# Optimization experiments

Measured on AMD Instinct MI355X. Metric: run time of the kernel, lower is better.

## Reference

```python
import jax, jax.numpy as jnp
import numpy as np

MODES = 32
WIDTH = 64


def crelu(z):
    # split-complex ReLU (torch.relu is undefined on complex; this is the standard fix)
    return jax.nn.relu(z.real) + 1j * jax.nn.relu(z.imag)


def _linear_params(key, fan_in, fan_out):
    k1, k2 = jax.random.split(key)
    s = 1.0 / np.sqrt(fan_in)
    W = jax.random.uniform(k1, (fan_out, fan_in), minval=-s, maxval=s, dtype=jnp.float32)
    b = jax.random.uniform(k2, (fan_out,), minval=-s, maxval=s, dtype=jnp.float32)
    return W, b


def setup_inputs() -> dict:
    key = jax.random.key(0)
    ks = jax.random.split(key, 8)
    B, G = 32768, 512
    H0, H1, H2 = 1024, 512, 64  # hidden_layers; H2 == WIDTH
    FD = 128                    # field_dim
    geometry_input = jax.random.normal(ks[0], (B, G), dtype=jnp.float32)
    W_in, b_in = _linear_params(ks[1], G, H0)
    W_h1, b_h1 = _linear_params(ks[2], H0, H1)
    W_h2, b_h2 = _linear_params(ks[3], H1, H2)
    w0 = jax.random.normal(ks[4], (MODES, WIDTH), dtype=jnp.float32)
    w1 = jax.random.normal(ks[5], (MODES, WIDTH), dtype=jnp.float32)
    lin1_W, lin1_b = _linear_params(ks[6], WIDTH, WIDTH)
    k7a, k7b = jax.random.split(ks[7])
    lin2_W, lin2_b = _linear_params(k7a, WIDTH, WIDTH)
    W_out, b_out = _linear_params(k7b, H2, FD)
    return dict(geometry_input=geometry_input, W_in=W_in, b_in=b_in,
                W_h1=W_h1, b_h1=b_h1, W_h2=W_h2, b_h2=b_h2,
                w0=w0, w1=w1, lin1_W=lin1_W, lin1_b=lin1_b,
                lin2_W=lin2_W, lin2_b=lin2_b, W_out=W_out, b_out=b_out)


def reference(geometry_input, W_in, b_in, W_h1, b_h1, W_h2, b_h2,
              w0, w1, lin1_W, lin1_b, lin2_W, lin2_b, W_out, b_out):
    # MLP encoder: [B, G] -> [B, 64]
    x = jax.nn.relu(geometry_input @ W_in.T + b_in)
    x = jax.nn.relu(x @ W_h1.T + b_h1)
    x = jax.nn.relu(x @ W_h2.T + b_h2)
    # FNO block
    xh = jnp.fft.fftn(x)  # fftn over ALL axes, as in torch code -> complex64 [B, 64]
    phase = jnp.exp(1j * 2.0 * jnp.pi * jnp.arange(MODES) / MODES).astype(jnp.complex64)
    y = xh[:, None, :] * w0  # per-mode lift: [B, MODES, WIDTH]
    y = crelu(y)
    y = y * phase[None, :, None]  # diagonal L mode-multiply
    y = jnp.einsum('bmw,mw->bw', y, w1.astype(y.dtype))  # collapse modes -> [B, WIDTH]
    y = crelu(y @ lin1_W.T + lin1_b)  # real weights on complex acts
    y = y @ lin2_W.T + lin2_b
    y = jnp.fft.ifftn(y)  # [B, 64] complex
    out = y @ W_out.T + b_out  # [B, field_dim] complex
    return out
```

## Files before the change

### kernel.cpp

```cpp
#include <hip/hip_runtime.h>
#include <hip/hip_bf16.h>


#define PI2F 6.28318530717958647692f

typedef __attribute__((ext_vector_type(8))) short short8;
typedef __attribute__((ext_vector_type(4))) float f32x4;

__device__ __forceinline__ unsigned short f2bf(float f) {
  unsigned int u = __float_as_uint(f);
  u += 0x7fff + ((u >> 16) & 1);
  return (unsigned short)(u >> 16);
}
__device__ __forceinline__ unsigned int pack_bf16x2(float a, float b) {
  return (unsigned int)f2bf(a) | ((unsigned int)f2bf(b) << 16);
}

__device__ __forceinline__ void gl2lds16(const void* gptr, const void* lptr) {
  __builtin_amdgcn_global_load_lds(
      (const __attribute__((address_space(1))) unsigned int*)(unsigned long long)gptr,
      (__attribute__((address_space(3))) unsigned int*)(unsigned int)(unsigned long long)lptr,
      16, 0, 0);
}

__global__ __launch_bounds__(256) void f32_to_bf16_k(
    const float* __restrict__ src, unsigned short* __restrict__ dst, int n4)
{
  int i = blockIdx.x * 256 + threadIdx.x;
  if (i < n4) {
    float4 v = ((const float4*)src)[i];
    uint2 p;
    p.x = pack_bf16x2(v.x, v.y);
    p.y = pack_bf16x2(v.z, v.w);
    ((uint2*)dst)[i] = p;
  }
}

template<int NBLOG, typename OUT>
__global__ __launch_bounds__(512, 1) void gemm_pipe(
    const unsigned short* __restrict__ A, const unsigned short* __restrict__ Bw,
    const float* __restrict__ bias, OUT* __restrict__ C, int N, int K)
{
  constexpr int BM = 128, BN = 256, BK = 64;
  constexpr int ASZ = BM * BK;
  constexpr int BSZ = BN * BK;
  constexpr int BUF = ASZ + BSZ;
  __shared__ __align__(16) unsigned short lds[3 * BUF];

  const int nwg = gridDim.x;
  const int cpx = nwg >> 3;
  const int orig = blockIdx.x;
  const int wg = (orig & 7) * cpx + (orig >> 3);
  const int mb = wg >> NBLOG;
  const int nb = wg & ((1 << NBLOG) - 1);
  const size_t m0 = (size_t)mb * BM;
  const size_t n0 = (size_t)nb * BN;

  const int tid = threadIdx.x;
  const int lane = tid & 63;
  const int wv = tid >> 6;
  const int q = lane >> 4, lr = lane & 15;
  const int x7 = lr & 7;
  const int wm = (wv >> 2) * 64;
  const int wn = (wv & 3) * 64;
  f32x4 acc[4][4] = {};

  auto STAGE_HALF = [&](int r, int kk, int s0) {
    unsigned short* dA = lds + r * BUF;
    #pragma unroll
    for (int u = 0; u < 3; ++u) {
      int e = wv * 6 + s0 + u;
      int isA = (e < 16) ? 1 : 0;
      int e2 = isA ? e : e - 16;
      int pc = e2 * 64 + lane;
      int row = pc >> 3, col = pc & 7;
      int lc = col ^ (row & 7);
      const unsigned short* src = isA ? A : Bw;
      size_t rb = isA ? m0 : n0;
      unsigned short* dst = dA + (isA ? 0 : ASZ) + e2 * 512;
      gl2lds16(src + (rb + row) * (size_t)K + kk + lc * 8, dst);
    }
  };

  const int nt = K / BK;
  STAGE_HALF(0, 0, 0); STAGE_HALF(0, 0, 3);
  STAGE_HALF(1, BK, 0); STAGE_HALF(1, BK, 3);
  asm volatile("s_waitcnt vmcnt(6)" ::: "memory");
  __builtin_amdgcn_s_barrier();

  int r0 = 0;
  for (int t = 0; t < nt; ++t) {
    const unsigned short* sA = lds + r0 * BUF;
    const unsigned short* sB = sA + ASZ;
    const bool st = (t + 2) < nt;
    const int r2 = (r0 >= 1) ? (r0 - 1) : 2;
    const int kk2 = (t + 2) * BK;

    short8 af[4][2], bf0[2][2];
    #pragma unroll
    for (int i = 0; i < 4; ++i)
      #pragma unroll
      for (int t2 = 0; t2 < 2; ++t2)
        af[i][t2] = *(const short8*)(sA + (wm + i * 16 + lr) * 64 + (((t2 << 2) | q) ^ x7) * 8);
    #pragma unroll
    for (int j = 0; j < 2; ++j)
      #pragma unroll
      for (int t2 = 0; t2 < 2; ++t2)
        bf0[j][t2] = *(const short8*)(sB + (wn + j * 16 + lr) * 64 + (((t2 << 2) | q) ^ x7) * 8);
    if (st) STAGE_HALF(r2, kk2, 0);
    __builtin_amdgcn_s_setprio(1);
    #pragma unroll
    for (int i = 0; i < 4; ++i)
      #pragma unroll
      for (int j = 0; j < 2; ++j)
        #pragma unroll
        for (int t2 = 0; t2 < 2; ++t2)
          acc[i][j] = __builtin_amdgcn_mfma_f32_16x16x32_bf16(af[i][t2], bf0[j][t2], acc[i][j], 0, 0, 0);
    __builtin_amdgcn_s_setprio(0);
    __builtin_amdgcn_s_barrier();

    short8 bf1[2][2];
    #pragma unroll
    for (int j = 0; j < 2; ++j)
      #pragma unroll
      for (int t2 = 0; t2 < 2; ++t2)
        bf1[j][t2] = *(const short8*)(sB + (wn + (j + 2) * 16 + lr) * 64 + (((t2 << 2) | q) ^ x7) * 8);
    if (st) STAGE_HALF(r2, kk2, 3);
    __builtin_amdgcn_s_setprio(1);
    #pragma unroll
    for (int i = 0; i < 4; ++i)
      #pragma unroll
      for (int j = 0; j < 2; ++j)
        #pragma unroll
        for (int t2 = 0; t2 < 2; ++t2)
          acc[i][j + 2] = __builtin_amdgcn_mfma_f32_16x16x32_bf16(af[i][t2], bf1[j][t2], acc[i][j + 2], 0, 0, 0);
    __builtin_amdgcn_s_setprio(0);

    asm volatile("s_waitcnt lgkmcnt(0)" ::: "memory");
    if (st) { asm volatile("s_waitcnt vmcnt(6)" ::: "memory"); }
    else    { asm volatile("s_waitcnt vmcnt(0)" ::: "memory"); }
    __builtin_amdgcn_s_barrier();
    r0 = (r0 + 1 >= 3) ? 0 : r0 + 1;
  }

  #pragma unroll
  for (int i = 0; i < 4; ++i)
    #pragma unroll
    for (int j = 0; j < 4; ++j) {
      size_t col = n0 + wn + j * 16 + lr;
      float bv = bias[col];
      #pragma unroll
      for (int r = 0; r < 4; ++r) {
        size_t row = m0 + wm + i * 16 + q * 4 + r;
        float v = acc[i][j][r] + bv;
        v = v > 0.f ? v : 0.f;
        if (sizeof(OUT) == 2) ((unsigned short*)C)[row * N + col] = f2bf(v);
        else                  ((float*)C)[row * N + col] = v;
      }
    }
}

template<int BM, int BN, int WM, int WN, typename OUT>
__global__ __launch_bounds__(256) void gemm_async(
    const unsigned short* __restrict__ A, const unsigned short* __restrict__ Bw,
    const float* __restrict__ bias, OUT* __restrict__ C,
    int M, int N, int K)
{
  constexpr int BK = 64;
  __shared__ __align__(16) unsigned short lA[BM * BK];
  __shared__ __align__(16) unsigned short lB[BN * BK];
  const int tid = threadIdx.x;
  const int lane = tid & 63;
  const int wv = tid >> 6;
  const int q = lane >> 4, lr = lane & 15;
  const int x7 = lr & 7;
  constexpr int WN_CNT = BN / WN;
  const int wm = (wv / WN_CNT) * WM;
  const int wn = (wv % WN_CNT) * WN;
  const size_t m0 = (size_t)blockIdx.x * BM;
  const size_t n0 = (size_t)blockIdx.y * BN;
  constexpr int MI = WM / 16, NI = WN / 16;
  f32x4 acc[MI][NI] = {};
  constexpr int A_INSTR = BM * BK / 512;
  constexpr int B_INSTR = BN * BK / 512;
  constexpr int A_PW = A_INSTR / 4, B_PW = B_INSTR / 4;
  (void)M;

  for (int k0 = 0; k0 < K; k0 += BK) {
    __syncthreads();
    #pragma unroll
    for (int s = 0; s < A_PW; ++s) {
      int instr = wv * A_PW + s;
      int pc = instr * 64 + lane;
      int row = pc >> 3, col = pc & 7;
      int lc = col ^ (row & 7);
      gl2lds16(A + (m0 + row) * K + k0 + lc * 8, lA + instr * 512);
    }
    #pragma unroll
    for (int s = 0; s < B_PW; ++s) {
      int instr = wv * B_PW + s;
      int pc = instr * 64 + lane;
      int row = pc >> 3, col = pc & 7;
      int lc = col ^ (row & 7);
      gl2lds16(Bw + (n0 + row) * K + k0 + lc * 8, lB + instr * 512);
    }
    __syncthreads();
    #pragma unroll
    for (int t = 0; t < 2; ++t) {
      short8 af[MI], bfr[NI];
      #pragma unroll
      for (int i = 0; i < MI; ++i) {
        int r = wm + i * 16 + lr;
        af[i] = *(const short8*)(lA + r * 64 + (((t << 2) | q) ^ x7) * 8);
      }
      #pragma unroll
      for (int j = 0; j < NI; ++j) {
        int r = wn + j * 16 + lr;
        bfr[j] = *(const short8*)(lB + r * 64 + (((t << 2) | q) ^ x7) * 8);
      }
      #pragma unroll
      for (int i = 0; i < MI; ++i)
        #pragma unroll
        for (int j = 0; j < NI; ++j)
          acc[i][j] = __builtin_amdgcn_mfma_f32_16x16x32_bf16(af[i], bfr[j], acc[i][j], 0, 0, 0);
    }
  }
  #pragma unroll
  for (int i = 0; i < MI; ++i)
    #pragma unroll
    for (int j = 0; j < NI; ++j) {
      size_t col = n0 + wn + j * 16 + lr;
      float bv = bias[col];
      #pragma unroll
      for (int r = 0; r < 4; ++r) {
        size_t row = m0 + wm + i * 16 + q * 4 + r;
        float v = acc[i][j][r] + bv;
        v = v > 0.f ? v : 0.f;
        if (sizeof(OUT) == 2) ((unsigned short*)C)[row * N + col] = f2bf(v);
        else                  ((float*)C)[row * N + col] = v;
      }
    }
}

__global__ __launch_bounds__(256) void precompute(
    const float* __restrict__ w0, const float* __restrict__ w1,
    const float* __restrict__ l2W, const float* __restrict__ l2b,
    float2* __restrict__ Ap, float2* __restrict__ Am,
    float2* __restrict__ Qt, float2* __restrict__ b2c)
{
  const int t = threadIdx.x;
  const int blk = blockIdx.x;
  if (blk == 0) {
    if (t < 64) {
      float apx = 0, apy = 0, amx = 0, amy = 0;
      for (int m = 0; m < 32; ++m) {
        float s0 = w0[m * 64 + t];
        float cf = w1[m * 64 + t] * s0;
        float sn, cs; sincosf(PI2F * (float)m / 32.f, &sn, &cs);
        if (s0 > 0.f)      { apx += cs * cf; apy += sn * cf; }
        else if (s0 < 0.f) { amx += cs * cf; amy += sn * cf; }
      }
      Ap[t] = make_float2(apx, apy);
      Am[t] = make_float2(amx, amy);
      float bx = 0, by = 0;
      for (int k = 0; k < 64; ++k) {
        float sn, cs; sincosf(PI2F * (float)((t * k) & 63) / 64.f, &sn, &cs);
        float lb = l2b[k] * (1.f / 64.f);
        bx += cs * lb; by += sn * lb;
      }
      b2c[t] = make_float2(bx, by);
    }
  } else {
    int e = (blk - 1) * 256 + t;
    int j = e >> 6, w = e & 63;
    float qx = 0, qy = 0;
    for (int k = 0; k < 64; ++k) {
      float sn, cs; sincosf(PI2F * (float)((j * k) & 63) / 64.f, &sn, &cs);
      float lw = l2W[k * 64 + w] * (1.f / 64.f);
      qx += cs * lw; qy += sn * lw;
    }
    Qt[w * 64 + j] = make_float2(qx, qy);
  }
}

__global__ __launch_bounds__(256) void dft64_rows(
    const float* __restrict__ x3, float2* __restrict__ xh1)
{
  __shared__ __align__(16) float xt[32][64];
  __shared__ float2 tw[64];
  const int t = threadIdx.x;
  const size_t b0 = (size_t)blockIdx.x * 32;
  for (int it = 0; it < 8; ++it) {
    int idx = it * 256 + t;
    int r = idx >> 6, w = idx & 63;
    xt[r][w] = x3[(b0 + r) * 64 + w];
  }
  if (t < 64) {
    float sn, cs; sincosf(-PI2F * (float)t / 64.f, &sn, &cs);
    tw[t] = make_float2(cs, sn);
  }
  __syncthreads();
  const int k = t & 63, rg = t >> 6;
  float2 acc[8] = {};
  #pragma unroll 1
  for (int w4 = 0; w4 < 16; ++w4) {
    int w = 4 * w4;
    int kw = k * w;
    float2 t0 = tw[kw & 63];
    float2 t1 = tw[(kw + k) & 63];
    float2 t2 = tw[(kw + 2 * k) & 63];
    float2 t3 = tw[(kw + 3 * k) & 63];
    #pragma unroll
    for (int r = 0; r < 8; ++r) {
      float4 xv = *(const float4*)(&xt[rg * 8 + r][w]);
      acc[r].x += xv.x * t0.x + xv.y * t1.x + xv.z * t2.x + xv.w * t3.x;
      acc[r].y += xv.x * t0.y + xv.y * t1.y + xv.z * t2.y + xv.w * t3.y;
    }
  }
  #pragma unroll
  for (int r = 0; r < 8; ++r)
    xh1[(b0 + rg * 8 + r) * 64 + k] = acc[r];
}

template<int SIGN>
__global__ __launch_bounds__(256) void fft_stage1(
    const float2* __restrict__ Xin, float2* __restrict__ T)
{
  __shared__ __align__(16) float2 tile[128 * 34];
  __shared__ float2 tw16s[16];
  const int blk = blockIdx.x;
  const int b2 = blk >> 1, wh = (blk & 1) * 32;
  const int t = threadIdx.x;
  #pragma unroll
  for (int it = 0; it < 8; ++it) {
    int idx = it * 256 + t;
    int b1 = idx >> 4, wi = (idx & 15) * 2;
    float4 v = *(const float4*)&Xin[((size_t)(b1 * 256 + b2)) * 64 + wh + wi];
    *(float4*)&tile[b1 * 34 + wi] = v;
  }
  if (t < 16) {
    float sn, cs; sincosf(SIGN * PI2F * (float)t / 16.f, &sn, &cs);
    tw16s[t] = make_float2(cs, sn);
  }
  __syncthreads();
  float2 twr[16];
  #pragma unroll
  for (int j = 0; j < 16; ++j) twr[j] = tw16s[j];

  {
    const int n2a = t >> 5, w = t & 31;
    float2 d[16];
    #pragma unroll
    for (int n1 = 0; n1 < 16; ++n1)
      d[n1] = tile[(8 * n1 + n2a) * 34 + w];
    float2 y[16];
    #pragma unroll
    for (int k = 0; k < 16; ++k) {
      float2 a = d[0];
      #pragma unroll
      for (int n1 = 1; n1 < 16; ++n1) {
        float2 tv = twr[(n1 * k) & 15];
        a.x += d[n1].x * tv.x - d[n1].y * tv.y;
        a.y += d[n1].x * tv.y + d[n1].y * tv.x;
      }
      y[k] = a;
    }
    float sstep, cstep;
    sincosf(SIGN * PI2F * (float)n2a / 128.f, &sstep, &cstep);
    float2 rot = make_float2(1.f, 0.f);
    #pragma unroll
    for (int k = 0; k < 16; ++k) {
      float2 a = y[k];
      y[k] = make_float2(a.x * rot.x - a.y * rot.y, a.x * rot.y + a.y * rot.x);
      float nrx = rot.x * cstep - rot.y * sstep;
      rot.y = rot.x * sstep + rot.y * cstep;
      rot.x = nrx;
    }
    __syncthreads();
    #pragma unroll
    for (int k = 0; k < 16; ++k)
      tile[(n2a * 16 + k) * 34 + w] = y[k];
  }
  __syncthreads();

  const int wB = t & 31, qB = t >> 5;
  float sstep, cstep;
  sincosf(SIGN * PI2F * (float)(16 * b2) / 32768.f, &sstep, &cstep);
  #pragma unroll
  for (int h = 0; h < 2; ++h) {
    const int k1p = qB + 8 * h;
    float2 d[8];
    #pragma unroll
    for (int n2 = 0; n2 < 8; ++n2)
      d[n2] = tile[(n2 * 16 + k1p) * 34 + wB];
    float2 acc[8];
    #pragma unroll
    for (int k2p = 0; k2p < 8; ++k2p) {
      float2 a = d[0];
      #pragma unroll
      for (int n2 = 1; n2 < 8; ++n2) {
        float2 tv = twr[(2 * n2 * k2p) & 15];
        a.x += d[n2].x * tv.x - d[n2].y * tv.y;
        a.y += d[n2].x * tv.y + d[n2].y * tv.x;
      }
      acc[k2p] = a;
    }
    float sb, cb;
    sincosf(SIGN * PI2F * (float)(b2 * k1p) / 32768.f, &sb, &cb);
    float2 rot = make_float2(cb, sb);
    #pragma unroll
    for (int k2p = 0; k2p < 8; ++k2p) {
      int k1 = k1p + 16 * k2p;
      float2 a = acc[k2p];
      T[((size_t)k1 * 256 + b2) * 64 + wh + wB] =
          make_float2(a.x * rot.x - a.y * rot.y, a.x * rot.y + a.y * rot.x);
      float nrx = rot.x * cstep - rot.y * sstep;
      rot.y = rot.x * sstep + rot.y * cstep;
      rot.x = nrx;
    }
  }
}

template<int SIGN, bool SCALE>
__global__ __launch_bounds__(256) void fft_stage2(
    const float2* __restrict__ T, float2* __restrict__ X)
{
  __shared__ __align__(16) float2 tile[256 * 18];
  __shared__ float2 tw16s[16];
  const int blk = blockIdx.x;
  const int k1 = blk >> 2, wq = (blk & 3) * 16;
  const int t = threadIdx.x;
  #pragma unroll
  for (int it = 0; it < 8; ++it) {
    int idx = it * 256 + t;
    int r2 = idx >> 3, wi = (idx & 7) * 2;
    float4 v = *(const float4*)&T[((size_t)k1 * 256 + r2) * 64 + wq + wi];
    *(float4*)&tile[r2 * 18 + wi] = v;
  }
  if (t < 16) {
    float sn, cs; sincosf(SIGN * PI2F * (float)t / 16.f, &sn, &cs);
    tw16s[t] = make_float2(cs, sn);
  }
  __syncthreads();
  float2 twr[16];
  #pragma unroll
  for (int j = 0; j < 16; ++j) twr[j] = tw16s[j];

  {
    const int n2a = t >> 4, w = t & 15;
    float2 d[16];
    #pragma unroll
    for (int n1 = 0; n1 < 16; ++n1)
      d[n1] = tile[(16 * n1 + n2a) * 18 + w];
    float2 y[16];
    #pragma unroll
    for (int k = 0; k < 16; ++k) {
      float2 a = d[0];
      #pragma unroll
      for (int n1 = 1; n1 < 16; ++n1) {
        float2 tv = twr[(n1 * k) & 15];
        a.x += d[n1].x * tv.x - d[n1].y * tv.y;
        a.y += d[n1].x * tv.y + d[n1].y * tv.x;
      }
      y[k] = a;
    }
    float sstep, cstep;
    sincosf(SIGN * PI2F * (float)n2a / 256.f, &sstep, &cstep);
    float2 rot = make_float2(1.f, 0.f);
    #pragma unroll
    for (int k = 0; k < 16; ++k) {
      float2 a = y[k];
      y[k] = make_float2(a.x * rot.x - a.y * rot.y, a.x * rot.y + a.y * rot.x);
      float nrx = rot.x * cstep - rot.y * sstep;
      rot.y = rot.x * sstep + rot.y * cstep;
      rot.x = nrx;
    }
    __syncthreads();
    #pragma unroll
    for (int k = 0; k < 16; ++k)
      tile[(n2a * 16 + k) * 18 + w] = y[k];
  }
  __syncthreads();

  const int k1pb = t >> 4, wB = t & 15;
  float2 d[16];
  #pragma unroll
  for (int n2 = 0; n2 < 16; ++n2)
    d[n2] = tile[(n2 * 16 + k1pb) * 18 + wB];
  const float sc = SCALE ? (1.f / 32768.f) : 1.f;
  #pragma unroll
  for (int k2p = 0; k2p < 16; ++k2p) {
    float2 a = d[0];
    #pragma unroll
    for (int n2 = 1; n2 < 16; ++n2) {
      float2 tv = twr[(n2 * k2p) & 15];
      a.x += d[n2].x * tv.x - d[n2].y * tv.y;
      a.y += d[n2].x * tv.y + d[n2].y * tv.x;
    }
    int k2 = k1pb + 16 * k2p;
    size_t row = (size_t)(k1 + 128 * k2);
    X[row * 64 + wq + wB] = make_float2(a.x * sc, a.y * sc);
  }
}

__global__ __launch_bounds__(256) void pw_lin(
    const float2* __restrict__ xh,
    const float2* __restrict__ Ap, const float2* __restrict__ Am,
    const float* __restrict__ l1W, const float* __restrict__ l1b,
    const float2* __restrict__ Qt, const float2* __restrict__ b2c,
    float2* __restrict__ u)
{
  __shared__ __align__(16) float2 tile[32][64];
  __shared__ __align__(16) float2 qt[64 * 64];
  const int t = threadIdx.x;
  const int lane = t & 63;
  const int wv = t >> 6;
  const size_t b0 = (size_t)blockIdx.x * 32;

  #pragma unroll
  for (int s = 0; s < 8; ++s) {
    int instr = wv * 8 + s;
    gl2lds16((const char*)Qt + instr * 1024 + lane * 16,
             (const char*)qt + instr * 1024);
  }

  for (int it = 0; it < 8; ++it) {
    int idx = it * 256 + t;
    int r = idx >> 6, w = idx & 63;
    float2 xv = xh[(b0 + r) * 64 + w];
    float2 Aa = (xv.x >= 0.f) ? Ap[w] : Am[w];
    float2 Ab = (xv.y >= 0.f) ? Ap[w] : Am[w];
    tile[r][w] = make_float2(xv.x * Aa.x - xv.y * Ab.y,
                             xv.x * Aa.y + xv.y * Ab.x);
  }
  __syncthreads();

  const int n = lane, rg = wv;

  {
    float2 acc[8] = {};
    const float* wrow = l1W + n * 64;
    float4 lwn = *(const float4*)wrow;
    #pragma unroll 1
    for (int w2 = 0; w2 < 16; ++w2) {
      float4 lw = lwn;
      lwn = *(const float4*)(wrow + 4 * ((w2 + 1) & 15));
      int w = 4 * w2;
      #pragma unroll
      for (int r = 0; r < 8; ++r) {
        const float4* rowp = (const float4*)(&tile[rg * 8 + r][w]);
        float4 y01 = rowp[0];
        float4 y23 = rowp[1];
        acc[r].x += y01.x * lw.x + y01.z * lw.y + y23.x * lw.z + y23.z * lw.w;
        acc[r].y += y01.y * lw.x + y01.w * lw.y + y23.y * lw.z + y23.w * lw.w;
      }
    }
    float bb = l1b[n];
    #pragma unroll
    for (int r = 0; r < 8; ++r) {
      float zr = acc[r].x + bb; zr = zr > 0.f ? zr : 0.f;
      float zi = acc[r].y;      zi = zi > 0.f ? zi : 0.f;
      tile[rg * 8 + r][n] = make_float2(zr, zi);
    }
  }

  {
    const int j = lane;
    float2 acc[8] = {};
    #pragma unroll 1
    for (int w2 = 0; w2 < 16; ++w2) {
      int w = 4 * w2;
      float2 q0 = qt[(w + 0) * 64 + j];
      float2 q1 = qt[(w + 1) * 64 + j];
      float2 q2 = qt[(w + 2) * 64 + j];
      float2 q3 = qt[(w + 3) * 64 + j];
      #pragma unroll
      for (int r = 0; r < 8; ++r) {
        const float4* rowp = (const float4*)(&tile[rg * 8 + r][w]);
        float4 z01 = rowp[0];
        float4 z23 = rowp[1];
        acc[r].x += z01.x * q0.x - z01.y * q0.y
                  + z01.z * q1.x - z01.w * q1.y
                  + z23.x * q2.x - z23.y * q2.y
                  + z23.z * q3.x - z23.w * q3.y;
        acc[r].y += z01.x * q0.y + z01.y * q0.x
                  + z01.z * q1.y + z01.w * q1.x
                  + z23.x * q2.y + z23.y * q2.x
                  + z23.z * q3.y + z23.w * q3.x;
      }
    }
    float2 bc = b2c[j];
    #pragma unroll
    for (int r = 0; r < 8; ++r)
      u[(b0 + rg * 8 + r) * 64 + j] = make_float2(acc[r].x + bc.x, acc[r].y + bc.y);
  }
}

template<int MODE>
__global__ __launch_bounds__(256) void final_out(
    const float2* __restrict__ v, const float* __restrict__ Wout,
    const float* __restrict__ bout, float* __restrict__ out)
{
  __shared__ __align__(16) float2 vt[32][64];
  const int t = threadIdx.x;
  const size_t b0 = (size_t)blockIdx.x * 32;
  for (int it = 0; it < 8; ++it) {
    int idx = it * 256 + t;
    int r = idx >> 6, w = idx & 63;
    vt[r][w] = v[(b0 + r) * 64 + w];
  }
  __syncthreads();
  const int f = t & 127, rg = t >> 7;
  const float* wrow = Wout + f * 64;
  float2 acc[16] = {};
  float2 wvn = *(const float2*)wrow;
  #pragma unroll 1
  for (int j2 = 0; j2 < 32; ++j2) {
    float2 wc = wvn;
    wvn = *(const float2*)(wrow + 2 * ((j2 + 1) & 31));
    #pragma unroll
    for (int r = 0; r < 16; ++r) {
      float4 vv = *(const float4*)(&vt[rg * 16 + r][2 * j2]);
      acc[r].x += vv.x * wc.x + vv.z * wc.y;
      acc[r].y += vv.y * wc.x + vv.w * wc.y;
    }
  }
  float bb = bout[f];
  #pragma unroll
  for (int r = 0; r < 16; ++r) {
    size_t idx = (b0 + rg * 16 + r) * 128 + f;
    if (MODE == 0) out[idx] = acc[r].x + bb;
    else ((float2*)out)[idx] = make_float2(acc[r].x + bb, acc[r].y);
  }
}

extern "C" void kernel_launch(void* const* d_in, const int* in_sizes, int n_in,
                              void* d_out, int out_size, void* d_ws, size_t ws_size,
                              hipStream_t stream)
{
  (void)in_sizes; (void)n_in; (void)ws_size;
  const float* geom = (const float*)d_in[0];
  const float* Win  = (const float*)d_in[1];
  const float* bin  = (const float*)d_in[2];
  const float* Wh1  = (const float*)d_in[3];
  const float* bh1  = (const float*)d_in[4];
  const float* Wh2  = (const float*)d_in[5];
  const float* bh2  = (const float*)d_in[6];
  const float* w0   = (const float*)d_in[7];
  const float* w1   = (const float*)d_in[8];
  const float* l1W  = (const float*)d_in[9];
  const float* l1b  = (const float*)d_in[10];
  const float* l2W  = (const float*)d_in[11];
  const float* l2b  = (const float*)d_in[12];
  const float* Wout = (const float*)d_in[13];
  const float* bout = (const float*)d_in[14];

  char* ws = (char*)d_ws;
  const size_t MB = 1048576ull;
  unsigned short* geomb = (unsigned short*)(ws);
  unsigned short* x2b   = (unsigned short*)(ws);
  unsigned short* x1b   = (unsigned short*)(ws + 32 * MB);
  float*  x3  = (float*)(ws + 32 * MB);
  float2* S0  = (float2*)(ws + 40 * MB);
  float2* S1  = (float2*)(ws + 56 * MB);
  float2* Ap  = (float2*)(ws + 72 * MB);
  float2* Am  = (float2*)(ws + 72 * MB + 512);
  float2* b2c = (float2*)(ws + 72 * MB + 1024);
  float2* Qt  = (float2*)(ws + 72 * MB + 1536);
  unsigned short* Winb = (unsigned short*)(ws + 96 * MB);
  unsigned short* Wh1b = (unsigned short*)(ws + 97 * MB);
  unsigned short* Wh2b = (unsigned short*)(ws + 98 * MB);

  f32_to_bf16_k<<<16384, 256, 0, stream>>>(geom, geomb, 4194304);
  f32_to_bf16_k<<<512, 256, 0, stream>>>(Win, Winb, 131072);
  f32_to_bf16_k<<<512, 256, 0, stream>>>(Wh1, Wh1b, 131072);
  f32_to_bf16_k<<<32, 256, 0, stream>>>(Wh2, Wh2b, 8192);

  gemm_pipe<2, unsigned short><<<1024, 512, 0, stream>>>(
      geomb, Winb, bin, x1b, 1024, 512);
  gemm_pipe<1, unsigned short><<<512, 512, 0, stream>>>(
      x1b, Wh1b, bh1, x2b, 512, 1024);
  gemm_async<128, 64,64,32,float><<<dim3(256, 1), 256, 0, stream>>>(
      x2b, Wh2b, bh2, x3, 32768, 64, 512);

  precompute<<<17, 256, 0, stream>>>(w0, w1, l2W, l2b, Ap, Am, Qt, b2c);
  dft64_rows<<<1024, 256, 0, stream>>>(x3, S0);
  fft_stage1<-1><<<512, 256, 0, stream>>>(S0, S1);
  fft_stage2<-1, false><<<512, 256, 0, stream>>>(S1, S0);
  pw_lin<<<1024, 256, 0, stream>>>(S0, Ap, Am, l1W, l1b, Qt, b2c, S1);
  fft_stage1<1><<<512, 256, 0, stream>>>(S1, S0);
  fft_stage2<1, true><<<512, 256, 0, stream>>>(S0, S1);
  if (out_size >= 8388608) {
    final_out<1><<<1024, 256, 0, stream>>>(S1, Wout, bout, (float*)d_out);
  } else {
    final_out<0><<<1024, 256, 0, stream>>>(S1, Wout, bout, (float*)d_out);
  }
}
```

Before: 414.9 us.

## Split GEMM main loop into four MFMA quadrant phases with interleaved staging

Restructures the bf16 GEMM inner loop from two phases into four phases, each computing a 2x2 quadrant of the 4x4 accumulator tile. Global-to-LDS staging is split into three pairs of loads spread across the phases, with barriers and lgkmcnt waits between them. The aim is to cut register pressure by holding fewer fragments at once and to spread memory traffic more evenly against MFMA work. The cost is extra barriers and a redundant reload of the A fragment rows in the last phase.

```diff
diff --git a/kernel.cpp b/kernel.cpp
--- a/kernel.cpp
+++ b/kernel.cpp
@@ -65,10 +65,10 @@
   const int wn = (wv & 3) * 64;
   f32x4 acc[4][4] = {};
 
-  auto STAGE_HALF = [&](int r, int kk, int s0) {
+  auto STAGE_PAIR = [&](int r, int kk, int s0) {
     unsigned short* dA = lds + r * BUF;
     #pragma unroll
-    for (int u = 0; u < 3; ++u) {
+    for (int u = 0; u < 2; ++u) {
       int e = wv * 6 + s0 + u;
       int isA = (e < 16) ? 1 : 0;
       int e2 = isA ? e : e - 16;
@@ -83,8 +83,8 @@
   };
 
   const int nt = K / BK;
-  STAGE_HALF(0, 0, 0); STAGE_HALF(0, 0, 3);
-  STAGE_HALF(1, BK, 0); STAGE_HALF(1, BK, 3);
+  STAGE_PAIR(0, 0, 0); STAGE_PAIR(0, 0, 2); STAGE_PAIR(0, 0, 4);
+  STAGE_PAIR(1, BK, 0); STAGE_PAIR(1, BK, 2); STAGE_PAIR(1, BK, 4);
   asm volatile("s_waitcnt vmcnt(6)" ::: "memory");
   __builtin_amdgcn_s_barrier();
 
@@ -96,47 +96,87 @@
     const int r2 = (r0 >= 1) ? (r0 - 1) : 2;
     const int kk2 = (t + 2) * BK;
 
-    short8 af[4][2], bf0[2][2];
-    #pragma unroll
-    for (int i = 0; i < 4; ++i)
+    short8 a0[2][2], a1[2][2], b0[2][2], b1[2][2];
+
+    #pragma unroll
+    for (int i = 0; i < 2; ++i)
       #pragma unroll
       for (int t2 = 0; t2 < 2; ++t2)
-        af[i][t2] = *(const short8*)(sA + (wm + i * 16 + lr) * 64 + (((t2 << 2) | q) ^ x7) * 8);
+        a0[i][t2] = *(const short8*)(sA + (wm + i * 16 + lr) * 64 + (((t2 << 2) | q) ^ x7) * 8);
     #pragma unroll
     for (int j = 0; j < 2; ++j)
       #pragma unroll
       for (int t2 = 0; t2 < 2; ++t2)
-        bf0[j][t2] = *(const short8*)(sB + (wn + j * 16 + lr) * 64 + (((t2 << 2) | q) ^ x7) * 8);
-    if (st) STAGE_HALF(r2, kk2, 0);
+        b0[j][t2] = *(const short8*)(sB + (wn + j * 16 + lr) * 64 + (((t2 << 2) | q) ^ x7) * 8);
+    if (st) STAGE_PAIR(r2, kk2, 0);
+    __builtin_amdgcn_s_barrier();
+    asm volatile("s_waitcnt lgkmcnt(0)" ::: "memory");
     __builtin_amdgcn_s_setprio(1);
     #pragma unroll
-    for (int i = 0; i < 4; ++i)
+    for (int i = 0; i < 2; ++i)
       #pragma unroll
       for (int j = 0; j < 2; ++j)
         #pragma unroll
         for (int t2 = 0; t2 < 2; ++t2)
-          acc[i][j] = __builtin_amdgcn_mfma_f32_16x16x32_bf16(af[i][t2], bf0[j][t2], acc[i][j], 0, 0, 0);
+          acc[i][j] = __builtin_amdgcn_mfma_f32_16x16x32_bf16(a0[i][t2], b0[j][t2], acc[i][j], 0, 0, 0);
     __builtin_amdgcn_s_setprio(0);
     __builtin_amdgcn_s_barrier();
 
-    short8 bf1[2][2];
-    #pragma unroll
-    for (int j = 0; j < 2; ++j)
+    #pragma unroll
+    for (int i = 0; i < 2; ++i)
       #pragma unroll
       for (int t2 = 0; t2 < 2; ++t2)
-        bf1[j][t2] = *(const short8*)(sB + (wn + (j + 2) * 16 + lr) * 64 + (((t2 << 2) | q) ^ x7) * 8);
-    if (st) STAGE_HALF(r2, kk2, 3);
+        a1[i][t2] = *(const short8*)(sA + (wm + (i + 2) * 16 + lr) * 64 + (((t2 << 2) | q) ^ x7) * 8);
+    if (st) STAGE_PAIR(r2, kk2, 2);
+    __builtin_amdgcn_s_barrier();
+    asm volatile("s_waitcnt lgkmcnt(0)" ::: "memory");
     __builtin_amdgcn_s_setprio(1);
     #pragma unroll
-    for (int i = 0; i < 4; ++i)
+    for (int i = 0; i < 2; ++i)
       #pragma unroll
       for (int j = 0; j < 2; ++j)
         #pragma unroll
         for (int t2 = 0; t2 < 2; ++t2)
-          acc[i][j + 2] = __builtin_amdgcn_mfma_f32_16x16x32_bf16(af[i][t2], bf1[j][t2], acc[i][j + 2], 0, 0, 0);
+          acc[i + 2][j] = __builtin_amdgcn_mfma_f32_16x16x32_bf16(a1[i][t2], b0[j][t2], acc[i + 2][j], 0, 0, 0);
     __builtin_amdgcn_s_setprio(0);
-
+    __builtin_amdgcn_s_barrier();
+
+    #pragma unroll
+    for (int j = 0; j < 2; ++j)
+      #pragma unroll
+      for (int t2 = 0; t2 < 2; ++t2)
+        b1[j][t2] = *(const short8*)(sB + (wn + (j + 2) * 16 + lr) * 64 + (((t2 << 2) | q) ^ x7) * 8);
+    if (st) STAGE_PAIR(r2, kk2, 4);
+    __builtin_amdgcn_s_barrier();
     asm volatile("s_waitcnt lgkmcnt(0)" ::: "memory");
+    __builtin_amdgcn_s_setprio(1);
+    #pragma unroll
+    for (int i = 0; i < 2; ++i)
+      #pragma unroll
+      for (int j = 0; j < 2; ++j)
+        #pragma unroll
+        for (int t2 = 0; t2 < 2; ++t2)
+          acc[i + 2][j + 2] = __builtin_amdgcn_mfma_f32_16x16x32_bf16(a1[i][t2], b1[j][t2], acc[i + 2][j + 2], 0, 0, 0);
+    __builtin_amdgcn_s_setprio(0);
+    __builtin_amdgcn_s_barrier();
+
+    #pragma unroll
+    for (int i = 0; i < 2; ++i)
+      #pragma unroll
+      for (int t2 = 0; t2 < 2; ++t2)
+        a0[i][t2] = *(const short8*)(sA + (wm + i * 16 + lr) * 64 + (((t2 << 2) | q) ^ x7) * 8);
+    __builtin_amdgcn_s_barrier();
+    asm volatile("s_waitcnt lgkmcnt(0)" ::: "memory");
+    __builtin_amdgcn_s_setprio(1);
+    #pragma unroll
+    for (int i = 0; i < 2; ++i)
+      #pragma unroll
+      for (int j = 0; j < 2; ++j)
+        #pragma unroll
+        for (int t2 = 0; t2 < 2; ++t2)
+          acc[i][j + 2] = __builtin_amdgcn_mfma_f32_16x16x32_bf16(a0[i][t2], b1[j][t2], acc[i][j + 2], 0, 0, 0);
+    __builtin_amdgcn_s_setprio(0);
+
     if (st) { asm volatile("s_waitcnt vmcnt(6)" ::: "memory"); }
     else    { asm volatile("s_waitcnt vmcnt(0)" ::: "memory"); }
     __builtin_amdgcn_s_barrier();
```

New measurement: 424.8 us. 2.4% more time.
